# Kernel tuning notes

Measured on AMD Instinct MI355X. Metric: run time of the kernel, lower is better.

The kernel has to match this reference:

```python
import jax, jax.numpy as jnp
import numpy as np
import math

B, T, D, H, DM = 2, 2048, 1024, 16, 256
DK = D // H

def setup_inputs() -> dict:
    key = jax.random.key(0)
    ks = jax.random.split(key, 13)
    s = 0.02
    return {
        "Hx": jax.random.normal(ks[0], (B, D, T, 1), jnp.float32),
        "Hf": jax.random.normal(ks[1], (B, T, D), jnp.float32),
        "Gm": jax.random.normal(ks[2], (B, T, DM), jnp.float32),
        "Wg": jax.random.normal(ks[3], (T, DM), jnp.float32) * s,
        "bg": jax.random.normal(ks[4], (T,), jnp.float32) * s,
        "Wq": jax.random.normal(ks[5], (D, 2 * D), jnp.float32) * s,
        "bq": jax.random.normal(ks[6], (D,), jnp.float32) * s,
        "Wk": jax.random.normal(ks[7], (D, 2 * D), jnp.float32) * s,
        "bk": jax.random.normal(ks[8], (D,), jnp.float32) * s,
        "Wv": jax.random.normal(ks[9], (D, D), jnp.float32) * s,
        "bv": jax.random.normal(ks[10], (D,), jnp.float32) * s,
        "Wo": jax.random.normal(ks[11], (D, D), jnp.float32) * s,
        "bo": jax.random.normal(ks[12], (D,), jnp.float32) * s,
    }

def reference(Hx, Hf, Gm, Wg, bg, Wq, bq, Wk, bk, Wv, bv, Wo, bo):
    # Hx: (B, D, T, 1) -> (B, T, D)
    hx = jnp.transpose(Hx[..., 0], (0, 2, 1))
    h_cat = jnp.concatenate([hx, Hf], axis=-1)          # (B, T, 2D)
    Q = h_cat @ Wq.T + bq                               # (B, T, D)
    K = h_cat @ Wk.T + bk
    V = hx @ Wv.T + bv
    # split heads: (B, H, T, DK)
    Q = Q.reshape(B, T, H, DK).transpose(0, 2, 1, 3)
    K = K.reshape(B, T, H, DK).transpose(0, 2, 1, 3)
    V = V.reshape(B, T, H, DK).transpose(0, 2, 1, 3)
    scores = jnp.einsum('bhqd,bhkd->bhqk', Q, K) / math.sqrt(DK)
    bias = Gm @ Wg.T + bg                                # (B, T, T)
    scores = scores + bias[:, None, :, :]
    attn = jax.nn.softmax(scores, axis=-1)
    out = jnp.einsum('bhqk,bhkd->bhqd', attn, V)
    out = out.transpose(0, 2, 1, 3).reshape(B, T, D)
    return out @ Wo.T + bo
```

## Files before the change

### kernel.cpp

```cpp
#include <hip/hip_runtime.h>
#include <hip/hip_bf16.h>

using bf16 = __hip_bfloat16;
typedef __attribute__((ext_vector_type(8))) __bf16 bf16x8;
typedef __attribute__((ext_vector_type(4))) float f32x4;

#define GLB_AS(p) ((const __attribute__((address_space(1))) unsigned int*)(p))
#define LDS_AS(p) ((__attribute__((address_space(3))) unsigned int*)(p))

__device__ __forceinline__ void async_copy16(const void* g, void* l) {
  __builtin_amdgcn_global_load_lds(GLB_AS(g), LDS_AS(l), 16, 0, 0);
}

__device__ __forceinline__ f32x4 mfma16x16x32(bf16x8 a, bf16x8 b, f32x4 c) {
  return __builtin_amdgcn_mfma_f32_16x16x32_bf16(a, b, c, 0, 0, 0);
}

__device__ __forceinline__ float bfu2f(unsigned short u) {
  union { unsigned int i; float f; } x;
  x.i = (unsigned int)u << 16;
  return x.f;
}

#define LOG2E 1.44269504f

__global__ __launch_bounds__(256) void pack_hx(const float* __restrict__ Hx,
                                               bf16* __restrict__ hcat) {
  __shared__ float tile[64][65];
  const int t0 = blockIdx.x * 64, d0 = blockIdx.y * 64, b = blockIdx.z;
  const int c = threadIdx.x & 63, r0 = threadIdx.x >> 6;
#pragma unroll
  for (int i = 0; i < 16; ++i) {
    const int rd = r0 + i * 4;
    tile[rd][c] = Hx[((size_t)(b * 1024 + d0 + rd)) * 2048 + t0 + c];
  }
  __syncthreads();
#pragma unroll
  for (int i = 0; i < 16; ++i) {
    const int ct = r0 + i * 4;
    hcat[((size_t)(b * 2048 + t0 + ct)) * 2048 + d0 + c] =
        __float2bfloat16(tile[c][ct]);
  }
}

__global__ __launch_bounds__(256) void pack_all(
    const float* __restrict__ Hf, const float* __restrict__ Wq,
    const float* __restrict__ Wk, const float* __restrict__ Wv,
    const float* __restrict__ Wo, const float* __restrict__ Wg,
    const float* __restrict__ Gm, const float* __restrict__ bq,
    const float* __restrict__ bk, const float* __restrict__ bv,
    bf16* __restrict__ hcat, bf16* __restrict__ Wqkvb, bf16* __restrict__ Wob,
    bf16* __restrict__ Wgb, bf16* __restrict__ Gmb,
    float* __restrict__ qkvbias) {
  const int gid = blockIdx.x * 256 + threadIdx.x;
  const float* src = nullptr;
  bf16* dst = nullptr;
  int lg = 0, ldo = 0, off = 0, idx = 0;
  bool zero = false;
  if (gid < 1048576) { idx = gid; src = Hf; dst = hcat; lg = 8; ldo = 2048; off = 1024; }
  else if (gid < 1572864) { idx = gid - 1048576; src = Wq; dst = Wqkvb; lg = 9; ldo = 2048; }
  else if (gid < 2097152) { idx = gid - 1572864; src = Wk; dst = Wqkvb + (size_t)1024 * 2048; lg = 9; ldo = 2048; }
  else if (gid < 2359296) { idx = gid - 2097152; src = Wv; dst = Wqkvb + (size_t)2048 * 2048; lg = 8; ldo = 2048; }
  else if (gid < 2621440) { idx = gid - 2359296; zero = true; dst = Wqkvb + (size_t)2048 * 2048 + 1024; lg = 8; ldo = 2048; }
  else if (gid < 2883584) { idx = gid - 2621440; src = Wo; dst = Wob; lg = 8; ldo = 1024; }
  else if (gid < 3014656) { idx = gid - 2883584; src = Wg; dst = Wgb; lg = 6; ldo = 256; }
  else if (gid < 3276800) { idx = gid - 3014656; src = Gm; dst = Gmb; lg = 6; ldo = 256; }
  else if (gid < 3277056) { const int i = gid - 3276800; ((float4*)qkvbias)[i] = ((const float4*)bq)[i]; return; }
  else if (gid < 3277312) { const int i = gid - 3277056; ((float4*)(qkvbias + 1024))[i] = ((const float4*)bk)[i]; return; }
  else { const int i = gid - 3277312; ((float4*)(qkvbias + 2048))[i] = ((const float4*)bv)[i]; return; }
  const int row = idx >> lg, c = idx & ((1 << lg) - 1);
  bf16* o = dst + (size_t)row * ldo + off + c * 4;
  __align__(8) bf16 tmp[4];
  if (zero) {
    tmp[0] = tmp[1] = tmp[2] = tmp[3] = __float2bfloat16(0.f);
  } else {
    const float4 v = ((const float4*)src)[(size_t)idx];
    tmp[0] = __float2bfloat16(v.x); tmp[1] = __float2bfloat16(v.y);
    tmp[2] = __float2bfloat16(v.z); tmp[3] = __float2bfloat16(v.w);
  }
  *(ushort4*)o = *(const ushort4*)tmp;
}

__global__ __launch_bounds__(256) void gemm_qkv_bias(
    const bf16* __restrict__ hcat, const bf16* __restrict__ Wqkv,
    const float* __restrict__ qkvbias, const bf16* __restrict__ Gmb,
    const bf16* __restrict__ Wgb, const float* __restrict__ bg,
    bf16* __restrict__ QKb, bf16* __restrict__ Vt, bf16* __restrict__ biasS) {
  __shared__ __align__(16) bf16 As[2][128 * 64];
  __shared__ __align__(16) bf16 Bs[2][128 * 64];
  const bool isqkv = blockIdx.x < 24;
  const bf16* A = isqkv ? hcat : Gmb;
  const bf16* W = isqkv ? Wqkv : Wgb;
  const float* biasv = isqkv ? qkvbias : bg;
  const int Kd = isqkv ? 2048 : 256;
  const int n0 = (isqkv ? blockIdx.x : (blockIdx.x - 24)) * 128;
  const int m0 = blockIdx.y * 128;
  const int tid = threadIdx.x, lane = tid & 63, w = tid >> 6;
  const int wm = (w >> 1) * 64, wn = (w & 1) * 64;
  const int fr = lane & 15;
  const int ck = lane >> 4;

  f32x4 acc[4][4];
  const f32x4 fzero = {0.f, 0.f, 0.f, 0.f};
#pragma unroll
  for (int i = 0; i < 4; ++i)
#pragma unroll
    for (int j = 0; j < 4; ++j) acc[i][j] = fzero;

  auto stage = [&](int it, int buf) {
    const int k0 = it * 64;
#pragma unroll
    for (int is = 0; is < 4; ++is) {
      const int off = is * 4096 + w * 1024;
      const int row = (off >> 7) + (lane >> 3);
      const int sch = ((lane & 7) ^ (row & 7)) * 8;
      async_copy16(A + (size_t)(m0 + row) * Kd + k0 + sch,
                   (char*)As[buf] + off);
      async_copy16(W + (size_t)(n0 + row) * Kd + k0 + sch,
                   (char*)Bs[buf] + off);
    }
  };

  const int nit = Kd >> 6;
  stage(0, 0);
  __syncthreads();
  for (int it = 0; it < nit; ++it) {
    const int cur = it & 1;
    if (it + 1 < nit) stage(it + 1, cur ^ 1);
#pragma unroll
    for (int ks = 0; ks < 2; ++ks) {
      bf16x8 af[4], bfr[4];
#pragma unroll
      for (int i = 0; i < 4; ++i) {
        const int swk = (((ks * 4 + ck) ^ (fr & 7))) * 8;
        af[i] = *(const bf16x8*)(As[cur] + (wm + i * 16 + fr) * 64 + swk);
        bfr[i] = *(const bf16x8*)(Bs[cur] + (wn + i * 16 + fr) * 64 + swk);
      }
#pragma unroll
      for (int i = 0; i < 4; ++i)
#pragma unroll
        for (int j = 0; j < 4; ++j)
          acc[i][j] = mfma16x16x32(af[i], bfr[j], acc[i][j]);
    }
    __syncthreads();
  }
  const int erow = (lane >> 4) * 4;
  const int ecol = lane & 15;

  if (!isqkv) {
#pragma unroll
    for (int i = 0; i < 4; ++i) {
      const int gm0 = m0 + wm + i * 16 + erow;
#pragma unroll
      for (int j = 0; j < 4; ++j) {
        const int gn = n0 + wn + j * 16 + ecol;
        const float bv = biasv[gn];
#pragma unroll
        for (int r = 0; r < 4; ++r)
          biasS[(size_t)(gm0 + r) * 2048 + gn] =
              __float2bfloat16((acc[i][j][r] + bv) * LOG2E);
      }
    }
  } else if (n0 < 2048) {
    const float sc = (n0 < 1024) ? 0.125f * LOG2E : 1.0f;
#pragma unroll
    for (int i = 0; i < 4; ++i) {
      const int gm0 = m0 + wm + i * 16 + erow;
#pragma unroll
      for (int j = 0; j < 4; ++j) {
        const int gn = n0 + wn + j * 16 + ecol;
        const float bv = biasv[gn];
#pragma unroll
        for (int r = 0; r < 4; ++r)
          QKb[(size_t)(gm0 + r) * 2048 + gn] =
              __float2bfloat16((acc[i][j][r] + bv) * sc);
      }
    }
  } else {
#pragma unroll
    for (int i = 0; i < 4; ++i) {
      const int gm0 = m0 + wm + i * 16 + erow;
      const int bb = gm0 >> 11;
      const int t = gm0 & 2047;
#pragma unroll
      for (int j = 0; j < 4; ++j) {
        const int gn = n0 + wn + j * 16 + ecol;
        const float bv = biasv[gn];
        const int d = gn - 2048;
        __align__(8) bf16 tmp[4];
#pragma unroll
        for (int r = 0; r < 4; ++r)
          tmp[r] = __float2bfloat16(acc[i][j][r] + bv);
        *(ushort4*)(Vt + ((size_t)(bb * 1024 + d)) * 2048 + t) =
            *(const ushort4*)tmp;
      }
    }
  }
}

__global__ __launch_bounds__(256) void gemm_out(const bf16* __restrict__ A,
                                                const bf16* __restrict__ W,
                                                const float* __restrict__ biasv,
                                                float* __restrict__ C) {
  __shared__ __align__(16) bf16 As[2][128 * 64];
  __shared__ __align__(16) bf16 Bs[2][64 * 64];
  const int tid = threadIdx.x, lane = tid & 63, w = tid >> 6;
  const int m0 = blockIdx.y * 128, n0 = blockIdx.x * 64;
  const int wm = (w >> 1) * 64, wn = (w & 1) * 32;
  const int fr = lane & 15;
  const int ck = lane >> 4;

  f32x4 acc[4][2];
  const f32x4 fzero = {0.f, 0.f, 0.f, 0.f};
#pragma unroll
  for (int i = 0; i < 4; ++i)
#pragma unroll
    for (int j = 0; j < 2; ++j) acc[i][j] = fzero;

  auto stage = [&](int it, int buf) {
    const int k0 = it * 64;
#pragma unroll
    for (int is = 0; is < 4; ++is) {
      const int off = is * 4096 + w * 1024;
      const int row = (off >> 7) + (lane >> 3);
      const int sch = ((lane & 7) ^ (row & 7)) * 8;
      async_copy16(A + (size_t)(m0 + row) * 1024 + k0 + sch,
                   (char*)As[buf] + off);
      if (is < 2)
        async_copy16(W + (size_t)(n0 + row) * 1024 + k0 + sch,
                     (char*)Bs[buf] + off);
    }
  };

  stage(0, 0);
  __syncthreads();
  for (int it = 0; it < 16; ++it) {
    const int cur = it & 1;
    if (it + 1 < 16) stage(it + 1, cur ^ 1);
#pragma unroll
    for (int ks = 0; ks < 2; ++ks) {
      bf16x8 af[4], bfr[2];
      const int swk0 = (((ks * 4 + ck) ^ (fr & 7))) * 8;
#pragma unroll
      for (int i = 0; i < 4; ++i)
        af[i] = *(const bf16x8*)(As[cur] + (wm + i * 16 + fr) * 64 + swk0);
#pragma unroll
      for (int j = 0; j < 2; ++j)
        bfr[j] = *(const bf16x8*)(Bs[cur] + (wn + j * 16 + fr) * 64 + swk0);
#pragma unroll
      for (int i = 0; i < 4; ++i)
#pragma unroll
        for (int j = 0; j < 2; ++j)
          acc[i][j] = mfma16x16x32(af[i], bfr[j], acc[i][j]);
    }
    __syncthreads();
  }
  const int erow = (lane >> 4) * 4;
  const int ecol = lane & 15;
#pragma unroll
  for (int i = 0; i < 4; ++i) {
    const int gm0 = m0 + wm + i * 16 + erow;
#pragma unroll
    for (int j = 0; j < 2; ++j) {
      const int gn = n0 + wn + j * 16 + ecol;
      const float bv = biasv[gn];
#pragma unroll
      for (int r = 0; r < 4; ++r)
        C[(size_t)(gm0 + r) * 1024 + gn] = acc[i][j][r] + bv;
    }
  }
}

__global__ __launch_bounds__(256) void flash_attn(
    const bf16* __restrict__ Qm, const bf16* __restrict__ Km,
    const bf16* __restrict__ Vtm, const bf16* __restrict__ biasS,
    bf16* __restrict__ Om) {
  __shared__ __align__(16) bf16 Ks[2][64 * 64];
  __shared__ __align__(16) bf16 Vs[2][64 * 64];
  __shared__ __align__(16) bf16 Ps[4 * 32 * 80];
  const int tid = threadIdx.x, lane = tid & 63, w = tid >> 6;
  const int q0 = blockIdx.x * 128;
  const int h = blockIdx.y, b = blockIdx.z;
  const int ql = lane & 15, qk = lane >> 4;
  const int T = 2048, D = 1024;
  const int sw0 = (qk ^ (ql & 7)) * 8;
  const int sw1 = ((qk + 4) ^ (ql & 7)) * 8;

  bf16x8 qf[2][2];
#pragma unroll
  for (int qt = 0; qt < 2; ++qt)
#pragma unroll
    for (int ks = 0; ks < 2; ++ks)
      qf[qt][ks] = *(const bf16x8*)(
          Qm + (size_t)(b * T + q0 + w * 32 + qt * 16 + ql) * 2048 + h * 64 +
          ks * 32 + qk * 8);

  f32x4 acc[4][2];
  const f32x4 fzero = {0.f, 0.f, 0.f, 0.f};
#pragma unroll
  for (int dt = 0; dt < 4; ++dt)
#pragma unroll
    for (int qt = 0; qt < 2; ++qt) acc[dt][qt] = fzero;
  float lp[2] = {0.f, 0.f};

  const bf16* kbase = Km + (size_t)(b * T) * 2048 + h * 64;
  const bf16* vbase = Vtm + (size_t)(b * D + h * 64) * 2048;
  const bf16* bb0 = biasS + (size_t)(b * T + q0 + w * 32 + ql) * 2048 + qk * 4;
  bf16* pb = Ps + w * 2560;

  auto stage = [&](int j, int buf) {
#pragma unroll
    for (int is = 0; is < 2; ++is) {
      const int off = is * 4096 + w * 1024;
      const int row = (off >> 7) + (lane >> 3);
      const int sch = ((lane & 7) ^ (row & 7)) * 8;
      async_copy16(kbase + (size_t)(j * 64 + row) * 2048 + sch,
                   (char*)Ks[buf] + off);
      async_copy16(vbase + (size_t)row * 2048 + j * 64 + sch,
                   (char*)Vs[buf] + off);
    }
  };

  ushort4 bq[2][4], bqn[2][4];
  stage(0, 0);
#pragma unroll
  for (int qt = 0; qt < 2; ++qt)
#pragma unroll
    for (int jt = 0; jt < 4; ++jt)
      bq[qt][jt] = *(const ushort4*)(bb0 + (size_t)qt * 16 * 2048 + jt * 16);
  __syncthreads();

  for (int j = 0; j < 32; ++j) {
    const int cur = j & 1;
    if (j < 31) {
      stage(j + 1, cur ^ 1);
#pragma unroll
      for (int qt = 0; qt < 2; ++qt)
#pragma unroll
        for (int jt = 0; jt < 4; ++jt)
          bqn[qt][jt] = *(const ushort4*)(bb0 + (size_t)qt * 16 * 2048 +
                                          (j + 1) * 64 + jt * 16);
    }
    const bf16* ksp = Ks[cur];
    const bf16* vsp = Vs[cur];
#pragma unroll
    for (int jt = 0; jt < 4; ++jt) {
      const bf16x8 kf0 = *(const bf16x8*)(ksp + (jt * 16 + ql) * 64 + sw0);
      const bf16x8 kf1 = *(const bf16x8*)(ksp + (jt * 16 + ql) * 64 + sw1);
#pragma unroll
      for (int qt = 0; qt < 2; ++qt) {
        f32x4 c;
        c[0] = bfu2f(bq[qt][jt].x); c[1] = bfu2f(bq[qt][jt].y);
        c[2] = bfu2f(bq[qt][jt].z); c[3] = bfu2f(bq[qt][jt].w);
        c = mfma16x16x32(kf0, qf[qt][0], c);
        c = mfma16x16x32(kf1, qf[qt][1], c);
        __align__(8) bf16 t4[4];
#pragma unroll
        for (int r = 0; r < 4; ++r) {
          const float pv = __builtin_amdgcn_exp2f(c[r]);
          lp[qt] += pv;
          t4[r] = __float2bfloat16(pv);
        }
        *(ushort4*)(pb + (qt * 16 + ql) * 80 + jt * 16 + qk * 4) =
            *(const ushort4*)t4;
      }
    }
#pragma unroll
    for (int ks = 0; ks < 2; ++ks) {
      const bf16x8 pf0 = *(const bf16x8*)(pb + ql * 80 + ks * 32 + qk * 8);
      const bf16x8 pf1 =
          *(const bf16x8*)(pb + (16 + ql) * 80 + ks * 32 + qk * 8);
      const int sw = ks ? sw1 : sw0;
#pragma unroll
      for (int dt = 0; dt < 4; ++dt) {
        const bf16x8 vf = *(const bf16x8*)(vsp + (dt * 16 + ql) * 64 + sw);
        acc[dt][0] = mfma16x16x32(pf0, vf, acc[dt][0]);
        acc[dt][1] = mfma16x16x32(pf1, vf, acc[dt][1]);
      }
    }
    if (j < 31) {
#pragma unroll
      for (int qt = 0; qt < 2; ++qt)
#pragma unroll
        for (int jt = 0; jt < 4; ++jt) bq[qt][jt] = bqn[qt][jt];
    }
    __syncthreads();
  }
#pragma unroll
  for (int qt = 0; qt < 2; ++qt) {
    lp[qt] += __shfl_xor(lp[qt], 16);
    lp[qt] += __shfl_xor(lp[qt], 32);
  }
  float inv[2][4];
#pragma unroll
  for (int qt = 0; qt < 2; ++qt)
#pragma unroll
    for (int r = 0; r < 4; ++r)
      inv[qt][r] = __builtin_amdgcn_rcpf(__shfl(lp[qt], qk * 4 + r));
#pragma unroll
  for (int qt = 0; qt < 2; ++qt)
#pragma unroll
    for (int r = 0; r < 4; ++r) {
      const size_t orow = (size_t)(b * T + q0 + w * 32 + qt * 16 + qk * 4 + r);
#pragma unroll
      for (int dt = 0; dt < 4; ++dt)
        Om[orow * D + h * 64 + dt * 16 + ql] =
            __float2bfloat16(acc[dt][qt][r] * inv[qt][r]);
    }
}

extern "C" void kernel_launch(void* const* d_in, const int* in_sizes, int n_in,
                              void* d_out, int out_size, void* d_ws,
                              size_t ws_size, hipStream_t stream) {
  (void)in_sizes; (void)n_in; (void)out_size; (void)ws_size;
  const float* Hx = (const float*)d_in[0];
  const float* Hf = (const float*)d_in[1];
  const float* Gm = (const float*)d_in[2];
  const float* Wg = (const float*)d_in[3];
  const float* bg = (const float*)d_in[4];
  const float* Wq = (const float*)d_in[5];
  const float* bq = (const float*)d_in[6];
  const float* Wk = (const float*)d_in[7];
  const float* bk = (const float*)d_in[8];
  const float* Wv = (const float*)d_in[9];
  const float* bv = (const float*)d_in[10];
  const float* Wo = (const float*)d_in[11];
  const float* bo = (const float*)d_in[12];
  float* out = (float*)d_out;

  char* p = (char*)d_ws;
  bf16* hcat = (bf16*)p;   p += (size_t)4096 * 2048 * 2;
  bf16* QKb = (bf16*)p;    p += (size_t)4096 * 2048 * 2;
  bf16* Vtb = (bf16*)p;    p += (size_t)4096 * 1024 * 2;
  bf16* biasS = (bf16*)p;  p += (size_t)4096 * 2048 * 2;
  bf16* AOut = (bf16*)p;   p += (size_t)4096 * 1024 * 2;
  bf16* Wqkvb = (bf16*)p;  p += (size_t)3072 * 2048 * 2;
  bf16* Wob = (bf16*)p;    p += (size_t)1024 * 1024 * 2;
  bf16* Wgb = (bf16*)p;    p += (size_t)2048 * 256 * 2;
  bf16* Gmb = (bf16*)p;    p += (size_t)4096 * 256 * 2;
  float* qkvbias = (float*)p; p += (size_t)3072 * 4;

  pack_hx<<<dim3(32, 16, 2), 256, 0, stream>>>(Hx, hcat);
  pack_all<<<dim3(12803), 256, 0, stream>>>(Hf, Wq, Wk, Wv, Wo, Wg, Gm, bq, bk,
                                            bv, hcat, Wqkvb, Wob, Wgb, Gmb,
                                            qkvbias);
  gemm_qkv_bias<<<dim3(40, 32), 256, 0, stream>>>(hcat, Wqkvb, qkvbias, Gmb,
                                                  Wgb, bg, QKb, Vtb, biasS);
  flash_attn<<<dim3(16, 16, 2), 256, 0, stream>>>(QKb, QKb + 1024, Vtb, biasS,
                                                  AOut);
  gemm_out<<<dim3(16, 32), 256, 0, stream>>>(AOut, Wob, bo, out);
}
```

Before: 298.9 us.

## Split attention over key halves with XCD-aware block mapping and combine kernel

```diff
diff --git a/kernel.cpp b/kernel.cpp
--- a/kernel.cpp
+++ b/kernel.cpp
@@ -88,13 +88,24 @@
     bf16* __restrict__ QKb, bf16* __restrict__ Vt, bf16* __restrict__ biasS) {
   __shared__ __align__(16) bf16 As[2][128 * 64];
   __shared__ __align__(16) bf16 Bs[2][128 * 64];
-  const bool isqkv = blockIdx.x < 24;
+  const int lin = blockIdx.x;
+  const int xcd = lin & 7;
+  const int kk = lin >> 3;
+  const bool isqkv = kk < 96;
+  int m_idx, n0;
+  if (isqkv) {
+    m_idx = kk / 3;
+    n0 = (xcd * 3 + (kk - m_idx * 3)) * 128;
+  } else {
+    const int k2 = kk - 96;
+    m_idx = k2 >> 1;
+    n0 = (xcd * 2 + (k2 & 1)) * 128;
+  }
+  const int m0 = m_idx * 128;
   const bf16* A = isqkv ? hcat : Gmb;
   const bf16* W = isqkv ? Wqkv : Wgb;
   const float* biasv = isqkv ? qkvbias : bg;
   const int Kd = isqkv ? 2048 : 256;
-  const int n0 = (isqkv ? blockIdx.x : (blockIdx.x - 24)) * 128;
-  const int m0 = blockIdx.y * 128;
   const int tid = threadIdx.x, lane = tid & 63, w = tid >> 6;
   const int wm = (w >> 1) * 64, wn = (w & 1) * 64;
   const int fr = lane & 15;
@@ -204,8 +215,12 @@
                                                 float* __restrict__ C) {
   __shared__ __align__(16) bf16 As[2][128 * 64];
   __shared__ __align__(16) bf16 Bs[2][64 * 64];
+  const int lin = blockIdx.x;
+  const int xcd = lin & 7;
+  const int kk = lin >> 3;
+  const int m0 = (kk >> 1) * 128;
+  const int n0 = (xcd * 2 + (kk & 1)) * 64;
   const int tid = threadIdx.x, lane = tid & 63, w = tid >> 6;
-  const int m0 = blockIdx.y * 128, n0 = blockIdx.x * 64;
   const int wm = (w >> 1) * 64, wn = (w & 1) * 32;
   const int fr = lane & 15;
   const int ck = lane >> 4;
@@ -274,13 +289,22 @@
 __global__ __launch_bounds__(256) void flash_attn(
     const bf16* __restrict__ Qm, const bf16* __restrict__ Km,
     const bf16* __restrict__ Vtm, const bf16* __restrict__ biasS,
-    bf16* __restrict__ Om) {
-  __shared__ __align__(16) bf16 Ks[2][64 * 64];
-  __shared__ __align__(16) bf16 Vs[2][64 * 64];
-  __shared__ __align__(16) bf16 Ps[4 * 32 * 80];
+    float* __restrict__ Op0, float* __restrict__ Op1,
+    float* __restrict__ lpart) {
+  __shared__ __align__(16) bf16 Ks[64 * 64];
+  __shared__ __align__(16) bf16 Vs[64 * 64];
+  __shared__ __align__(16) bf16 Ps[4 * 32 * 72];
+  const int lin = blockIdx.x;
+  const int xcd = lin & 7;
+  const int kk = lin >> 3;
+  const int cl = kk & 3;
+  const int r2 = kk >> 2;
+  const int half = r2 & 1;
+  const int q0 = (r2 >> 1) * 128;
+  const int combo = xcd * 4 + cl;
+  const int h = combo & 15;
+  const int b = combo >> 4;
   const int tid = threadIdx.x, lane = tid & 63, w = tid >> 6;
-  const int q0 = blockIdx.x * 128;
-  const int h = blockIdx.y, b = blockIdx.z;
   const int ql = lane & 15, qk = lane >> 4;
   const int T = 2048, D = 1024;
   const int sw0 = (qk ^ (ql & 7)) * 8;
@@ -306,47 +330,32 @@
   const bf16* kbase = Km + (size_t)(b * T) * 2048 + h * 64;
   const bf16* vbase = Vtm + (size_t)(b * D + h * 64) * 2048;
   const bf16* bb0 = biasS + (size_t)(b * T + q0 + w * 32 + ql) * 2048 + qk * 4;
-  bf16* pb = Ps + w * 2560;
-
-  auto stage = [&](int j, int buf) {
+  bf16* pb = Ps + w * 2304;
+
+  for (int j = 0; j < 16; ++j) {
+    const int jj = half * 16 + j;
+    __syncthreads();
 #pragma unroll
     for (int is = 0; is < 2; ++is) {
       const int off = is * 4096 + w * 1024;
       const int row = (off >> 7) + (lane >> 3);
       const int sch = ((lane & 7) ^ (row & 7)) * 8;
-      async_copy16(kbase + (size_t)(j * 64 + row) * 2048 + sch,
-                   (char*)Ks[buf] + off);
-      async_copy16(vbase + (size_t)row * 2048 + j * 64 + sch,
-                   (char*)Vs[buf] + off);
-    }
-  };
-
-  ushort4 bq[2][4], bqn[2][4];
-  stage(0, 0);
-#pragma unroll
-  for (int qt = 0; qt < 2; ++qt)
-#pragma unroll
-    for (int jt = 0; jt < 4; ++jt)
-      bq[qt][jt] = *(const ushort4*)(bb0 + (size_t)qt * 16 * 2048 + jt * 16);
-  __syncthreads();
-
-  for (int j = 0; j < 32; ++j) {
-    const int cur = j & 1;
-    if (j < 31) {
-      stage(j + 1, cur ^ 1);
-#pragma unroll
-      for (int qt = 0; qt < 2; ++qt)
-#pragma unroll
-        for (int jt = 0; jt < 4; ++jt)
-          bqn[qt][jt] = *(const ushort4*)(bb0 + (size_t)qt * 16 * 2048 +
-                                          (j + 1) * 64 + jt * 16);
-    }
-    const bf16* ksp = Ks[cur];
-    const bf16* vsp = Vs[cur];
+      async_copy16(kbase + (size_t)(jj * 64 + row) * 2048 + sch,
+                   (char*)Ks + off);
+      async_copy16(vbase + (size_t)row * 2048 + jj * 64 + sch, (char*)Vs + off);
+    }
+    ushort4 bq[2][4];
+#pragma unroll
+    for (int qt = 0; qt < 2; ++qt)
+#pragma unroll
+      for (int jt = 0; jt < 4; ++jt)
+        bq[qt][jt] = *(const ushort4*)(bb0 + (size_t)qt * 16 * 2048 + jj * 64 +
+                                       jt * 16);
+    __syncthreads();
 #pragma unroll
     for (int jt = 0; jt < 4; ++jt) {
-      const bf16x8 kf0 = *(const bf16x8*)(ksp + (jt * 16 + ql) * 64 + sw0);
-      const bf16x8 kf1 = *(const bf16x8*)(ksp + (jt * 16 + ql) * 64 + sw1);
+      const bf16x8 kf0 = *(const bf16x8*)(Ks + (jt * 16 + ql) * 64 + sw0);
+      const bf16x8 kf1 = *(const bf16x8*)(Ks + (jt * 16 + ql) * 64 + sw1);
 #pragma unroll
       for (int qt = 0; qt < 2; ++qt) {
         f32x4 c;
@@ -361,42 +370,36 @@
           lp[qt] += pv;
           t4[r] = __float2bfloat16(pv);
         }
-        *(ushort4*)(pb + (qt * 16 + ql) * 80 + jt * 16 + qk * 4) =
+        *(ushort4*)(pb + (qt * 16 + ql) * 72 + jt * 16 + qk * 4) =
             *(const ushort4*)t4;
       }
     }
 #pragma unroll
     for (int ks = 0; ks < 2; ++ks) {
-      const bf16x8 pf0 = *(const bf16x8*)(pb + ql * 80 + ks * 32 + qk * 8);
+      const bf16x8 pf0 = *(const bf16x8*)(pb + ql * 72 + ks * 32 + qk * 8);
       const bf16x8 pf1 =
-          *(const bf16x8*)(pb + (16 + ql) * 80 + ks * 32 + qk * 8);
+          *(const bf16x8*)(pb + (16 + ql) * 72 + ks * 32 + qk * 8);
       const int sw = ks ? sw1 : sw0;
 #pragma unroll
       for (int dt = 0; dt < 4; ++dt) {
-        const bf16x8 vf = *(const bf16x8*)(vsp + (dt * 16 + ql) * 64 + sw);
+        const bf16x8 vf = *(const bf16x8*)(Vs + (dt * 16 + ql) * 64 + sw);
         acc[dt][0] = mfma16x16x32(pf0, vf, acc[dt][0]);
         acc[dt][1] = mfma16x16x32(pf1, vf, acc[dt][1]);
       }
     }
-    if (j < 31) {
-#pragma unroll
-      for (int qt = 0; qt < 2; ++qt)
-#pragma unroll
-        for (int jt = 0; jt < 4; ++jt) bq[qt][jt] = bqn[qt][jt];
-    }
-    __syncthreads();
   }
 #pragma unroll
   for (int qt = 0; qt < 2; ++qt) {
     lp[qt] += __shfl_xor(lp[qt], 16);
     lp[qt] += __shfl_xor(lp[qt], 32);
   }
-  float inv[2][4];
-#pragma unroll
-  for (int qt = 0; qt < 2; ++qt)
-#pragma unroll
-    for (int r = 0; r < 4; ++r)
-      inv[qt][r] = __builtin_amdgcn_rcpf(__shfl(lp[qt], qk * 4 + r));
+  if (qk == 0) {
+#pragma unroll
+    for (int qt = 0; qt < 2; ++qt)
+      lpart[half * 65536 + (b * 16 + h) * 2048 + q0 + w * 32 + qt * 16 + ql] =
+          lp[qt];
+  }
+  float* Op = half ? Op1 : Op0;
 #pragma unroll
   for (int qt = 0; qt < 2; ++qt)
 #pragma unroll
@@ -404,9 +407,26 @@
       const size_t orow = (size_t)(b * T + q0 + w * 32 + qt * 16 + qk * 4 + r);
 #pragma unroll
       for (int dt = 0; dt < 4; ++dt)
-        Om[orow * D + h * 64 + dt * 16 + ql] =
-            __float2bfloat16(acc[dt][qt][r] * inv[qt][r]);
-    }
+        Op[orow * 1024 + h * 64 + dt * 16 + ql] = acc[dt][qt][r];
+    }
+}
+
+__global__ __launch_bounds__(256) void combine(const float* __restrict__ O0,
+                                               const float* __restrict__ O1,
+                                               const float* __restrict__ lpart,
+                                               bf16* __restrict__ AOut) {
+  const int idx = blockIdx.x * 256 + threadIdx.x;
+  const int row = idx >> 8;
+  const int col = (idx & 255) * 4;
+  const int b = row >> 11, q = row & 2047, h = col >> 6;
+  const int li = (b * 16 + h) * 2048 + q;
+  const float inv = __builtin_amdgcn_rcpf(lpart[li] + lpart[65536 + li]);
+  const float4 a = *(const float4*)(O0 + (size_t)row * 1024 + col);
+  const float4 c = *(const float4*)(O1 + (size_t)row * 1024 + col);
+  __align__(8) bf16 t[4] = {
+      __float2bfloat16((a.x + c.x) * inv), __float2bfloat16((a.y + c.y) * inv),
+      __float2bfloat16((a.z + c.z) * inv), __float2bfloat16((a.w + c.w) * inv)};
+  *(ushort4*)(AOut + (size_t)row * 1024 + col) = *(const ushort4*)t;
 }
 
 extern "C" void kernel_launch(void* const* d_in, const int* in_sizes, int n_in,
@@ -439,14 +459,18 @@
   bf16* Wgb = (bf16*)p;    p += (size_t)2048 * 256 * 2;
   bf16* Gmb = (bf16*)p;    p += (size_t)4096 * 256 * 2;
   float* qkvbias = (float*)p; p += (size_t)3072 * 4;
+  float* Op1 = (float*)p;  p += (size_t)4096 * 1024 * 4;
+  float* lpart = (float*)p; p += (size_t)2 * 65536 * 4;
+  float* Op0 = (float*)hcat;
 
   pack_hx<<<dim3(32, 16, 2), 256, 0, stream>>>(Hx, hcat);
   pack_all<<<dim3(12803), 256, 0, stream>>>(Hf, Wq, Wk, Wv, Wo, Wg, Gm, bq, bk,
                                             bv, hcat, Wqkvb, Wob, Wgb, Gmb,
                                             qkvbias);
-  gemm_qkv_bias<<<dim3(40, 32), 256, 0, stream>>>(hcat, Wqkvb, qkvbias, Gmb,
-                                                  Wgb, bg, QKb, Vtb, biasS);
-  flash_attn<<<dim3(16, 16, 2), 256, 0, stream>>>(QKb, QKb + 1024, Vtb, biasS,
-                                                  AOut);
-  gemm_out<<<dim3(16, 32), 256, 0, stream>>>(AOut, Wob, bo, out);
-}
+  gemm_qkv_bias<<<dim3(1280), 256, 0, stream>>>(hcat, Wqkvb, qkvbias, Gmb,
+                                                Wgb, bg, QKb, Vtb, biasS);
+  flash_attn<<<dim3(1024), 256, 0, stream>>>(QKb, QKb + 1024, Vtb, biasS,
+                                             Op0, Op1, lpart);
+  combine<<<dim3(4096), 256, 0, stream>>>(Op0, Op1, lpart, AOut);
+  gemm_out<<<dim3(512), 256, 0, stream>>>(AOut, Wob, bo, out);
+}
```

New measurement: 306.3 us. +2.5%, slower.
